# Optimization experiments

Measured on AMD Instinct MI355X. Metric: run time of the kernel, lower is better.

Reference implementation:

```python
import jax, jax.numpy as jnp
import numpy as np


def _topk_masked_softmax(attn, k):
    # Keep only the top-k entries per row (last dim), softmax over them.
    _, idx = jax.lax.top_k(attn, k)  # [b, nh, C, k]
    mask = jnp.put_along_axis(
        jnp.zeros(attn.shape, dtype=bool), idx, True, axis=-1, inplace=False
    )
    return jax.nn.softmax(jnp.where(mask, attn, -jnp.inf), axis=-1)


def setup_inputs() -> dict:
    key = jax.random.key(0)
    k0, k1, k2, k3, k4 = jax.random.split(key, 5)
    b, nh, C = 8, 8, 512
    attn = jax.random.normal(k0, (b, nh, C, C), dtype=jnp.float32)
    # In the torch module these are Parameters initialized to 0.2; use random
    # positive scalars of similar scale for a non-degenerate baseline.
    w1 = jax.random.uniform(k1, (1,), dtype=jnp.float32)
    w2 = jax.random.uniform(k2, (1,), dtype=jnp.float32)
    w3 = jax.random.uniform(k3, (1,), dtype=jnp.float32)
    w4 = jax.random.uniform(k4, (1,), dtype=jnp.float32)
    return {"attn": attn, "w1": w1, "w2": w2, "w3": w3, "w4": w4}


def reference(attn, w1, w2, w3, w4):
    C = attn.shape[-1]
    a1 = _topk_masked_softmax(attn, int(C / 2))
    a2 = _topk_masked_softmax(attn, int(C * 2 / 3))
    a3 = _topk_masked_softmax(attn, int(C * 3 / 4))
    a4 = _topk_masked_softmax(attn, int(C * 4 / 5))
    return a1 * w1 + a2 * w2 + a3 * w3 + a4 * w4
```

## Files before the change

kernel.cpp:

```cpp
#include <hip/hip_runtime.h>
#include <math.h>

#define ROW_C 512
#define NBIN 2048
#define NPACK (NBIN / 2)


static __device__ __forceinline__ unsigned scan64_add(unsigned v) {
    int x = (int)v;
    x += __builtin_amdgcn_update_dpp(0, x, 0x111, 0xF, 0xF, false);
    x += __builtin_amdgcn_update_dpp(0, x, 0x112, 0xF, 0xF, false);
    x += __builtin_amdgcn_update_dpp(0, x, 0x114, 0xF, 0xE, false);
    x += __builtin_amdgcn_update_dpp(0, x, 0x118, 0xF, 0xC, false);
    x += __builtin_amdgcn_update_dpp(0, x, 0x142, 0xA, 0xF, false);
    x += __builtin_amdgcn_update_dpp(0, x, 0x143, 0xC, 0xF, false);
    return (unsigned)x;
}

static __device__ __forceinline__ unsigned scan16_add(unsigned v) {
    int x = (int)v;
    x += __builtin_amdgcn_update_dpp(0, x, 0x111, 0xF, 0xF, false);
    x += __builtin_amdgcn_update_dpp(0, x, 0x112, 0xF, 0xF, false);
    x += __builtin_amdgcn_update_dpp(0, x, 0x114, 0xF, 0xE, false);
    x += __builtin_amdgcn_update_dpp(0, x, 0x118, 0xF, 0xC, false);
    return (unsigned)x;
}

static __device__ __forceinline__ float wave_fadd_red(float v) {
    float t;
    t = __int_as_float(__builtin_amdgcn_update_dpp(0, __float_as_int(v), 0x111, 0xF, 0xF, false)); v += t;
    t = __int_as_float(__builtin_amdgcn_update_dpp(0, __float_as_int(v), 0x112, 0xF, 0xF, false)); v += t;
    t = __int_as_float(__builtin_amdgcn_update_dpp(0, __float_as_int(v), 0x114, 0xF, 0xE, false)); v += t;
    t = __int_as_float(__builtin_amdgcn_update_dpp(0, __float_as_int(v), 0x118, 0xF, 0xC, false)); v += t;
    t = __int_as_float(__builtin_amdgcn_update_dpp(0, __float_as_int(v), 0x142, 0xA, 0xF, false)); v += t;
    t = __int_as_float(__builtin_amdgcn_update_dpp(0, __float_as_int(v), 0x143, 0xC, 0xF, false)); v += t;
    return __int_as_float(__builtin_amdgcn_readlane(__float_as_int(v), 63));
}

static __device__ __forceinline__ float wave_fmax_red(float v) {
    const int NI = (int)0xFF800000;
    float t;
    t = __int_as_float(__builtin_amdgcn_update_dpp(NI, __float_as_int(v), 0x111, 0xF, 0xF, false)); v = fmaxf(v, t);
    t = __int_as_float(__builtin_amdgcn_update_dpp(NI, __float_as_int(v), 0x112, 0xF, 0xF, false)); v = fmaxf(v, t);
    t = __int_as_float(__builtin_amdgcn_update_dpp(NI, __float_as_int(v), 0x114, 0xF, 0xE, false)); v = fmaxf(v, t);
    t = __int_as_float(__builtin_amdgcn_update_dpp(NI, __float_as_int(v), 0x118, 0xF, 0xC, false)); v = fmaxf(v, t);
    t = __int_as_float(__builtin_amdgcn_update_dpp(NI, __float_as_int(v), 0x142, 0xA, 0xF, false)); v = fmaxf(v, t);
    t = __int_as_float(__builtin_amdgcn_update_dpp(NI, __float_as_int(v), 0x143, 0xC, 0xF, false)); v = fmaxf(v, t);
    return __int_as_float(__builtin_amdgcn_readlane(__float_as_int(v), 63));
}

__global__ __launch_bounds__(256) void topk_ms_kernel(
    const float* __restrict__ attn,
    const float* __restrict__ w1p, const float* __restrict__ w2p,
    const float* __restrict__ w3p, const float* __restrict__ w4p,
    float* __restrict__ out)
{
    __shared__ __align__(16) unsigned hist_all[4][NPACK];

    const int lane = threadIdx.x & 63;
    const int wv   = threadIdx.x >> 6;
    unsigned* h = hist_all[wv];
    int4* hv = (int4*)h;

    const long long row  = (long long)blockIdx.x * 4 + wv;
    const long long base = row * ROW_C + lane * 8;

    const float4 A = *reinterpret_cast<const float4*>(attn + base);
    const float4 B = *reinterpret_cast<const float4*>(attn + base + 4);
    float x[8] = {A.x, A.y, A.z, A.w, B.x, B.y, B.z, B.w};

    int bin[8];
    float eo[8];
    #pragma unroll
    for (int s = 0; s < 8; ++s) {
        const float y = __builtin_amdgcn_fmed3f(x[s], -3.90625f, 3.90625f) + 12.0f;
        bin[s] = (int)((__float_as_uint(y) >> 12) & 0x7FFu);
        eo[s] = __expf(x[s]);
    }

    {
        const int4 z = make_int4(0, 0, 0, 0);
        hv[lane] = z; hv[lane + 64] = z; hv[lane + 128] = z; hv[lane + 192] = z;
    }

    #pragma unroll
    for (int s = 0; s < 8; ++s) {
        const int j  = bin[s] >> 1;
        const int ph = j ^ ((j >> 3) & 0x1C);
        atomicAdd(&h[ph], (bin[s] & 1) ? 0x10000u : 1u);
    }

    unsigned ps = 0;
    #pragma unroll
    for (int k = 0; k < 4; ++k) {
        const int b  = 4 * lane + k;
        const int pb = b ^ ((b >> 3) & 7);
        const int4 v = hv[pb];
        ps += (unsigned)v.x + (unsigned)v.y + (unsigned)v.z + (unsigned)v.w;
    }
    const unsigned tot = (ps & 0xFFFFu) + (ps >> 16);

    const unsigned incl = scan64_add(tot);
    const unsigned excl = incl - tot;

    const unsigned long long Ba = __ballot(incl >= 257u);
    const unsigned long long Bb = __ballot(incl >= 172u);
    const unsigned long long Bc = __ballot(incl >= 129u);
    const unsigned long long Bd = __ballot(incl >= 104u);
    const int l0 = __ffsll(Ba) - 1, l1 = __ffsll(Bb) - 1,
              l2 = __ffsll(Bc) - 1, l3 = __ffsll(Bd) - 1;

    const int r = lane >> 4;
    const int lsel = (r == 0) ? l0 : (r == 1) ? l1 : (r == 2) ? l2 : l3;
    const int Tr   = (r == 0) ? 257 : (r == 1) ? 172 : (r == 2) ? 129 : 104;
    const int Kr   = (r == 0) ? 256 : (r == 1) ? 341 : (r == 2) ? 384 : 409;
    const unsigned exl = __shfl(excl, lsel, 64);

    const int jw = (lsel << 4) + (lane & 15);
    const int pw = jw ^ ((jw >> 3) & 0x1C);
    const unsigned w0 = h[pw];
    const unsigned q  = w0 + (w0 << 16);
    const unsigned wt = q >> 16;
    const unsigned sc = scan16_add(wt);
    const unsigned ebase = exl + (sc - wt);
    const int      phi   = (int)(ebase + wt);
    const unsigned long long CB = __ballot(phi >= Tr);
    const int js = __ffs((unsigned)(CB >> (r << 4))) - 1;
    const unsigned q_w  = __shfl(q, (r << 4) + js, 64);
    const unsigned eb_w = __shfl(ebase, (r << 4) + js, 64);

    const int  plo  = (int)(eb_w + (q_w & 0xFFFFu));
    const int  phw  = (int)(eb_w + (q_w >> 16));
    const bool ev   = (plo >= Tr);
    const int  bsel = (((lsel << 4) + js) << 1) + (ev ? 0 : 1);
    const int  locp = ev ? plo : phw;
    const int  prvp = ev ? (int)eb_w : plo;
    const int  Rr   = Kr - 512 + locp;
    const int  alin = (prvp == Tr - 1) ? 1 : 0;
    const unsigned pk = ((unsigned)bsel << 11) | ((unsigned)alin << 10) | (unsigned)Rr;

    int b_[4], R_[4], al_[4]; float tthr[4];
    const float NINF = -__builtin_inff();
    {
        const unsigned v0 = (unsigned)__builtin_amdgcn_readlane((int)pk, 0);
        const unsigned v1 = (unsigned)__builtin_amdgcn_readlane((int)pk, 16);
        const unsigned v2 = (unsigned)__builtin_amdgcn_readlane((int)pk, 32);
        const unsigned v3 = (unsigned)__builtin_amdgcn_readlane((int)pk, 48);
        const unsigned vv[4] = {v0, v1, v2, v3};
        #pragma unroll
        for (int rr = 0; rr < 4; ++rr) {
            b_[rr]  = (int)(vv[rr] >> 11);
            al_[rr] = (int)((vv[rr] >> 10) & 1u);
            R_[rr]  = (int)(vv[rr] & 0x3FFu);
            float t = __uint_as_float((unsigned)(b_[rr] + 0x41000) << 12) - 12.0f;
            tthr[rr] = (b_[rr] <= 24) ? NINF : t;
        }
    }

    int needv[4] = {0,0,0,0}, cntv[4] = {0,0,0,0};
    bool anytb = false;
    #pragma unroll
    for (int rr = 0; rr < 4; ++rr) {
        if (!al_[rr]) {
            float cm[8];
            #pragma unroll
            for (int s = 0; s < 8; ++s)
                cm[s] = (bin[s] == b_[rr]) ? x[s] : NINF;
            int R = R_[rr];
            float t; int c;
            while (true) {
                float mk = cm[0];
                #pragma unroll
                for (int s = 1; s < 8; ++s) mk = fmaxf(mk, cm[s]);
                t = wave_fmax_red(mk);
                c = 0;
                #pragma unroll
                for (int s = 0; s < 8; ++s)
                    c += (int)__popcll(__ballot(cm[s] == t));
                if (c >= R) break;
                R -= c;
                #pragma unroll
                for (int s = 0; s < 8; ++s)
                    cm[s] = (cm[s] == t) ? NINF : cm[s];
            }
            tthr[rr] = t; needv[rr] = R; cntv[rr] = c;
            anytb = anytb || (c != R);
        }
    }

    float res[8];
    if (!anytb) {
        const float t1 = tthr[0], t2 = tthr[1], t3 = tthr[2], t4 = tthr[3];
        float z0 = 0.f, z1 = 0.f, z2 = 0.f, z3 = 0.f;
        #pragma unroll
        for (int s = 0; s < 8; ++s) {
            z0 += (x[s] >= t1) ? eo[s] : 0.f;
            z1 += (x[s] >= t2) ? eo[s] : 0.f;
            z2 += (x[s] >= t3) ? eo[s] : 0.f;
            z3 += (x[s] >= t4) ? eo[s] : 0.f;
        }
        const float Z0 = wave_fadd_red(z0);
        const float Z1 = wave_fadd_red(z1);
        const float Z2 = wave_fadd_red(z2);
        const float Z3 = wave_fadd_red(z3);
        const float wz0 = w1p[0] * __builtin_amdgcn_rcpf(Z0);
        const float wz1 = w2p[0] * __builtin_amdgcn_rcpf(Z1);
        const float wz2 = w3p[0] * __builtin_amdgcn_rcpf(Z2);
        const float wz3 = w4p[0] * __builtin_amdgcn_rcpf(Z3);
        const float u4 = wz3, u3 = u4 + wz2, u2 = u3 + wz1, u1 = u2 + wz0;
        #pragma unroll
        for (int s = 0; s < 8; ++s) {
            float c = (x[s] >= t1) ? u1 : u2;
            c = (x[s] >= t2) ? c : u3;
            c = (x[s] >= t3) ? c : u4;
            c = (x[s] >= t4) ? c : 0.f;
            res[s] = eo[s] * c;
        }
    } else {
        int fl[8] = {0, 0, 0, 0, 0, 0, 0, 0};
        #pragma unroll
        for (int rr = 0; rr < 4; ++rr) {
            const float t = tthr[rr];
            if (al_[rr] || needv[rr] == cntv[rr]) {
                #pragma unroll
                for (int s = 0; s < 8; ++s)
                    fl[s] |= ((int)(x[s] >= t)) << rr;
            } else {
                const unsigned long long ltm = (1ull << lane) - 1ull;
                int basec = 0;
                #pragma unroll
                for (int s = 0; s < 8; ++s)
                    basec += (int)__popcll(__ballot(x[s] == t) & ltm);
                int own = 0;
                #pragma unroll
                for (int s = 0; s < 8; ++s) {
                    const bool eq = (x[s] == t);
                    if (x[s] > t || (eq && (basec + own) < needv[rr]))
                        fl[s] |= (1 << rr);
                    own += eq ? 1 : 0;
                }
            }
        }
        float z0 = 0.f, z1 = 0.f, z2 = 0.f, z3 = 0.f;
        #pragma unroll
        for (int s = 0; s < 8; ++s) {
            z0 += (fl[s] & 1) ? eo[s] : 0.f;
            z1 += (fl[s] & 2) ? eo[s] : 0.f;
            z2 += (fl[s] & 4) ? eo[s] : 0.f;
            z3 += (fl[s] & 8) ? eo[s] : 0.f;
        }
        const float Z0 = wave_fadd_red(z0);
        const float Z1 = wave_fadd_red(z1);
        const float Z2 = wave_fadd_red(z2);
        const float Z3 = wave_fadd_red(z3);
        const float wz0 = w1p[0] * __builtin_amdgcn_rcpf(Z0);
        const float wz1 = w2p[0] * __builtin_amdgcn_rcpf(Z1);
        const float wz2 = w3p[0] * __builtin_amdgcn_rcpf(Z2);
        const float wz3 = w4p[0] * __builtin_amdgcn_rcpf(Z3);
        #pragma unroll
        for (int s = 0; s < 8; ++s) {
            float c = 0.f;
            c += (fl[s] & 1) ? wz0 : 0.f;
            c += (fl[s] & 2) ? wz1 : 0.f;
            c += (fl[s] & 4) ? wz2 : 0.f;
            c += (fl[s] & 8) ? wz3 : 0.f;
            res[s] = eo[s] * c;
        }
    }

    *reinterpret_cast<float4*>(out + base)     = make_float4(res[0], res[1], res[2], res[3]);
    *reinterpret_cast<float4*>(out + base + 4) = make_float4(res[4], res[5], res[6], res[7]);
}

extern "C" void kernel_launch(void* const* d_in, const int* in_sizes, int n_in,
                              void* d_out, int out_size, void* d_ws, size_t ws_size,
                              hipStream_t stream) {
    const float* attn = (const float*)d_in[0];
    const float* w1   = (const float*)d_in[1];
    const float* w2   = (const float*)d_in[2];
    const float* w3   = (const float*)d_in[3];
    const float* w4   = (const float*)d_in[4];
    float* out = (float*)d_out;

    int rows = in_sizes[0] / ROW_C;
    int blocks = (rows + 3) / 4;
    topk_ms_kernel<<<blocks, 256, 0, stream>>>(attn, w1, w2, w3, w4, out);
}
```

Before: 122.3 us.

## Process two rows per wavefront and interleave histogram and threshold phases

```diff
diff --git a/kernel.cpp b/kernel.cpp
--- a/kernel.cpp
+++ b/kernel.cpp
@@ -62,86 +62,93 @@
     unsigned* h = hist_all[wv];
     int4* hv = (int4*)h;
 
-    const long long row  = (long long)blockIdx.x * 4 + wv;
-    const long long base = row * ROW_C + lane * 8;
-
-    const float4 A = *reinterpret_cast<const float4*>(attn + base);
-    const float4 B = *reinterpret_cast<const float4*>(attn + base + 4);
-    float x[8] = {A.x, A.y, A.z, A.w, B.x, B.y, B.z, B.w};
-
-    int bin[8];
-    float eo[8];
-    #pragma unroll
-    for (int s = 0; s < 8; ++s) {
-        const float y = __builtin_amdgcn_fmed3f(x[s], -3.90625f, 3.90625f) + 12.0f;
-        bin[s] = (int)((__float_as_uint(y) >> 12) & 0x7FFu);
-        eo[s] = __expf(x[s]);
+    const long long gid   = (long long)blockIdx.x * 4 + wv;
+    const long long baseA = gid * (2 * ROW_C) + lane * 8;
+    const long long baseB = baseA + ROW_C;
+
+    float xA[8], xB[8];
+    {
+        const float4 A0 = *reinterpret_cast<const float4*>(attn + baseA);
+        const float4 A1 = *reinterpret_cast<const float4*>(attn + baseA + 4);
+        const float4 B0 = *reinterpret_cast<const float4*>(attn + baseB);
+        const float4 B1 = *reinterpret_cast<const float4*>(attn + baseB + 4);
+        xA[0]=A0.x; xA[1]=A0.y; xA[2]=A0.z; xA[3]=A0.w;
+        xA[4]=A1.x; xA[5]=A1.y; xA[6]=A1.z; xA[7]=A1.w;
+        xB[0]=B0.x; xB[1]=B0.y; xB[2]=B0.z; xB[3]=B0.w;
+        xB[4]=B1.x; xB[5]=B1.y; xB[6]=B1.z; xB[7]=B1.w;
     }
 
-    {
+    const float NINF = -__builtin_inff();
+
+    auto BINF = [](float v) -> int {
+        const float y = __builtin_amdgcn_fmed3f(v, -3.90625f, 3.90625f) + 12.0f;
+        return (int)((__float_as_uint(y) >> 12) & 0x7FFu);
+    };
+
+    auto ZERO = [&]() {
         const int4 z = make_int4(0, 0, 0, 0);
         hv[lane] = z; hv[lane + 64] = z; hv[lane + 128] = z; hv[lane + 192] = z;
-    }
-
-    #pragma unroll
-    for (int s = 0; s < 8; ++s) {
-        const int j  = bin[s] >> 1;
-        const int ph = j ^ ((j >> 3) & 0x1C);
-        atomicAdd(&h[ph], (bin[s] & 1) ? 0x10000u : 1u);
-    }
-
-    unsigned ps = 0;
-    #pragma unroll
-    for (int k = 0; k < 4; ++k) {
-        const int b  = 4 * lane + k;
-        const int pb = b ^ ((b >> 3) & 7);
-        const int4 v = hv[pb];
-        ps += (unsigned)v.x + (unsigned)v.y + (unsigned)v.z + (unsigned)v.w;
-    }
-    const unsigned tot = (ps & 0xFFFFu) + (ps >> 16);
-
-    const unsigned incl = scan64_add(tot);
-    const unsigned excl = incl - tot;
-
-    const unsigned long long Ba = __ballot(incl >= 257u);
-    const unsigned long long Bb = __ballot(incl >= 172u);
-    const unsigned long long Bc = __ballot(incl >= 129u);
-    const unsigned long long Bd = __ballot(incl >= 104u);
-    const int l0 = __ffsll(Ba) - 1, l1 = __ffsll(Bb) - 1,
-              l2 = __ffsll(Bc) - 1, l3 = __ffsll(Bd) - 1;
-
-    const int r = lane >> 4;
-    const int lsel = (r == 0) ? l0 : (r == 1) ? l1 : (r == 2) ? l2 : l3;
-    const int Tr   = (r == 0) ? 257 : (r == 1) ? 172 : (r == 2) ? 129 : 104;
-    const int Kr   = (r == 0) ? 256 : (r == 1) ? 341 : (r == 2) ? 384 : 409;
-    const unsigned exl = __shfl(excl, lsel, 64);
-
-    const int jw = (lsel << 4) + (lane & 15);
-    const int pw = jw ^ ((jw >> 3) & 0x1C);
-    const unsigned w0 = h[pw];
-    const unsigned q  = w0 + (w0 << 16);
-    const unsigned wt = q >> 16;
-    const unsigned sc = scan16_add(wt);
-    const unsigned ebase = exl + (sc - wt);
-    const int      phi   = (int)(ebase + wt);
-    const unsigned long long CB = __ballot(phi >= Tr);
-    const int js = __ffs((unsigned)(CB >> (r << 4))) - 1;
-    const unsigned q_w  = __shfl(q, (r << 4) + js, 64);
-    const unsigned eb_w = __shfl(ebase, (r << 4) + js, 64);
-
-    const int  plo  = (int)(eb_w + (q_w & 0xFFFFu));
-    const int  phw  = (int)(eb_w + (q_w >> 16));
-    const bool ev   = (plo >= Tr);
-    const int  bsel = (((lsel << 4) + js) << 1) + (ev ? 0 : 1);
-    const int  locp = ev ? plo : phw;
-    const int  prvp = ev ? (int)eb_w : plo;
-    const int  Rr   = Kr - 512 + locp;
-    const int  alin = (prvp == Tr - 1) ? 1 : 0;
-    const unsigned pk = ((unsigned)bsel << 11) | ((unsigned)alin << 10) | (unsigned)Rr;
-
-    int b_[4], R_[4], al_[4]; float tthr[4];
-    const float NINF = -__builtin_inff();
-    {
+    };
+
+    auto HIST = [&](const float* x) {
+        #pragma unroll
+        for (int s = 0; s < 8; ++s) {
+            const int b  = BINF(x[s]);
+            const int j  = b >> 1;
+            const int ph = j ^ ((j >> 3) & 0x1C);
+            atomicAdd(&h[ph], (b & 1) ? 0x10000u : 1u);
+        }
+    };
+
+    auto FRONT = [&](float* tthr, int* b_, int* R_, int* al_) {
+        unsigned ps = 0;
+        #pragma unroll
+        for (int k = 0; k < 4; ++k) {
+            const int b  = 4 * lane + k;
+            const int pb = b ^ ((b >> 3) & 7);
+            const int4 v = hv[pb];
+            ps += (unsigned)v.x + (unsigned)v.y + (unsigned)v.z + (unsigned)v.w;
+        }
+        const unsigned tot  = (ps & 0xFFFFu) + (ps >> 16);
+        const unsigned incl = scan64_add(tot);
+        const unsigned excl = incl - tot;
+
+        const unsigned long long Ba = __ballot(incl >= 257u);
+        const unsigned long long Bb = __ballot(incl >= 172u);
+        const unsigned long long Bc = __ballot(incl >= 129u);
+        const unsigned long long Bd = __ballot(incl >= 104u);
+        const int l0 = __ffsll(Ba) - 1, l1 = __ffsll(Bb) - 1,
+                  l2 = __ffsll(Bc) - 1, l3 = __ffsll(Bd) - 1;
+
+        const int r = lane >> 4;
+        const int lsel = (r == 0) ? l0 : (r == 1) ? l1 : (r == 2) ? l2 : l3;
+        const int Tr   = (r == 0) ? 257 : (r == 1) ? 172 : (r == 2) ? 129 : 104;
+        const int Kr   = (r == 0) ? 256 : (r == 1) ? 341 : (r == 2) ? 384 : 409;
+        const unsigned exl = __shfl(excl, lsel, 64);
+
+        const int jw = (lsel << 4) + (lane & 15);
+        const int pw = jw ^ ((jw >> 3) & 0x1C);
+        const unsigned w0 = h[pw];
+        const unsigned q  = w0 + (w0 << 16);
+        const unsigned wt = q >> 16;
+        const unsigned sc = scan16_add(wt);
+        const unsigned ebase = exl + (sc - wt);
+        const int      phi   = (int)(ebase + wt);
+        const unsigned long long CB = __ballot(phi >= Tr);
+        const int js = __ffs((unsigned)(CB >> (r << 4))) - 1;
+        const unsigned q_w  = __shfl(q, (r << 4) + js, 64);
+        const unsigned eb_w = __shfl(ebase, (r << 4) + js, 64);
+
+        const int  plo  = (int)(eb_w + (q_w & 0xFFFFu));
+        const int  phw  = (int)(eb_w + (q_w >> 16));
+        const bool ev   = (plo >= Tr);
+        const int  bsel = (((lsel << 4) + js) << 1) + (ev ? 0 : 1);
+        const int  locp = ev ? plo : phw;
+        const int  prvp = ev ? (int)eb_w : plo;
+        const int  Rr   = Kr - 512 + locp;
+        const int  alin = (prvp == Tr - 1) ? 1 : 0;
+        const unsigned pk = ((unsigned)bsel << 11) | ((unsigned)alin << 10) | (unsigned)Rr;
+
         const unsigned v0 = (unsigned)__builtin_amdgcn_readlane((int)pk, 0);
         const unsigned v1 = (unsigned)__builtin_amdgcn_readlane((int)pk, 16);
         const unsigned v2 = (unsigned)__builtin_amdgcn_readlane((int)pk, 32);
@@ -155,121 +162,147 @@
             float t = __uint_as_float((unsigned)(b_[rr] + 0x41000) << 12) - 12.0f;
             tthr[rr] = (b_[rr] <= 24) ? NINF : t;
         }
-    }
-
-    int needv[4] = {0,0,0,0}, cntv[4] = {0,0,0,0};
-    bool anytb = false;
-    #pragma unroll
-    for (int rr = 0; rr < 4; ++rr) {
-        if (!al_[rr]) {
-            float cm[8];
-            #pragma unroll
-            for (int s = 0; s < 8; ++s)
-                cm[s] = (bin[s] == b_[rr]) ? x[s] : NINF;
-            int R = R_[rr];
-            float t; int c;
-            while (true) {
-                float mk = cm[0];
-                #pragma unroll
-                for (int s = 1; s < 8; ++s) mk = fmaxf(mk, cm[s]);
-                t = wave_fmax_red(mk);
-                c = 0;
+    };
+
+    auto BACK = [&](const float* x, float* tthr, const int* b_, const int* R_,
+                    const int* al_, long long obase) {
+        int needv[4] = {0,0,0,0}, cntv[4] = {0,0,0,0};
+        bool anytb = false;
+        const bool needbins = !(al_[0] && al_[1] && al_[2] && al_[3]);
+        int bn[8];
+        if (needbins) {
+            #pragma unroll
+            for (int s = 0; s < 8; ++s) bn[s] = BINF(x[s]);
+        }
+        #pragma unroll
+        for (int rr = 0; rr < 4; ++rr) {
+            if (!al_[rr]) {
+                float cm[8];
                 #pragma unroll
                 for (int s = 0; s < 8; ++s)
-                    c += (int)__popcll(__ballot(cm[s] == t));
-                if (c >= R) break;
-                R -= c;
-                #pragma unroll
-                for (int s = 0; s < 8; ++s)
-                    cm[s] = (cm[s] == t) ? NINF : cm[s];
-            }
-            tthr[rr] = t; needv[rr] = R; cntv[rr] = c;
-            anytb = anytb || (c != R);
-        }
-    }
-
-    float res[8];
-    if (!anytb) {
-        const float t1 = tthr[0], t2 = tthr[1], t3 = tthr[2], t4 = tthr[3];
-        float z0 = 0.f, z1 = 0.f, z2 = 0.f, z3 = 0.f;
-        #pragma unroll
-        for (int s = 0; s < 8; ++s) {
-            z0 += (x[s] >= t1) ? eo[s] : 0.f;
-            z1 += (x[s] >= t2) ? eo[s] : 0.f;
-            z2 += (x[s] >= t3) ? eo[s] : 0.f;
-            z3 += (x[s] >= t4) ? eo[s] : 0.f;
-        }
-        const float Z0 = wave_fadd_red(z0);
-        const float Z1 = wave_fadd_red(z1);
-        const float Z2 = wave_fadd_red(z2);
-        const float Z3 = wave_fadd_red(z3);
-        const float wz0 = w1p[0] * __builtin_amdgcn_rcpf(Z0);
-        const float wz1 = w2p[0] * __builtin_amdgcn_rcpf(Z1);
-        const float wz2 = w3p[0] * __builtin_amdgcn_rcpf(Z2);
-        const float wz3 = w4p[0] * __builtin_amdgcn_rcpf(Z3);
-        const float u4 = wz3, u3 = u4 + wz2, u2 = u3 + wz1, u1 = u2 + wz0;
-        #pragma unroll
-        for (int s = 0; s < 8; ++s) {
-            float c = (x[s] >= t1) ? u1 : u2;
-            c = (x[s] >= t2) ? c : u3;
-            c = (x[s] >= t3) ? c : u4;
-            c = (x[s] >= t4) ? c : 0.f;
-            res[s] = eo[s] * c;
-        }
-    } else {
-        int fl[8] = {0, 0, 0, 0, 0, 0, 0, 0};
-        #pragma unroll
-        for (int rr = 0; rr < 4; ++rr) {
-            const float t = tthr[rr];
-            if (al_[rr] || needv[rr] == cntv[rr]) {
-                #pragma unroll
-                for (int s = 0; s < 8; ++s)
-                    fl[s] |= ((int)(x[s] >= t)) << rr;
-            } else {
-                const unsigned long long ltm = (1ull << lane) - 1ull;
-                int basec = 0;
-                #pragma unroll
-                for (int s = 0; s < 8; ++s)
-                    basec += (int)__popcll(__ballot(x[s] == t) & ltm);
-                int own = 0;
-                #pragma unroll
-                for (int s = 0; s < 8; ++s) {
-                    const bool eq = (x[s] == t);
-                    if (x[s] > t || (eq && (basec + own) < needv[rr]))
-                        fl[s] |= (1 << rr);
-                    own += eq ? 1 : 0;
+                    cm[s] = (bn[s] == b_[rr]) ? x[s] : NINF;
+                int R = R_[rr];
+                float t; int c;
+                while (true) {
+                    float mk = cm[0];
+                    #pragma unroll
+                    for (int s = 1; s < 8; ++s) mk = fmaxf(mk, cm[s]);
+                    t = wave_fmax_red(mk);
+                    c = 0;
+                    #pragma unroll
+                    for (int s = 0; s < 8; ++s)
+                        c += (int)__popcll(__ballot(cm[s] == t));
+                    if (c >= R) break;
+                    R -= c;
+                    #pragma unroll
+                    for (int s = 0; s < 8; ++s)
+                        cm[s] = (cm[s] == t) ? NINF : cm[s];
                 }
-            }
-        }
-        float z0 = 0.f, z1 = 0.f, z2 = 0.f, z3 = 0.f;
-        #pragma unroll
-        for (int s = 0; s < 8; ++s) {
-            z0 += (fl[s] & 1) ? eo[s] : 0.f;
-            z1 += (fl[s] & 2) ? eo[s] : 0.f;
-            z2 += (fl[s] & 4) ? eo[s] : 0.f;
-            z3 += (fl[s] & 8) ? eo[s] : 0.f;
-        }
-        const float Z0 = wave_fadd_red(z0);
-        const float Z1 = wave_fadd_red(z1);
-        const float Z2 = wave_fadd_red(z2);
-        const float Z3 = wave_fadd_red(z3);
-        const float wz0 = w1p[0] * __builtin_amdgcn_rcpf(Z0);
-        const float wz1 = w2p[0] * __builtin_amdgcn_rcpf(Z1);
-        const float wz2 = w3p[0] * __builtin_amdgcn_rcpf(Z2);
-        const float wz3 = w4p[0] * __builtin_amdgcn_rcpf(Z3);
-        #pragma unroll
-        for (int s = 0; s < 8; ++s) {
-            float c = 0.f;
-            c += (fl[s] & 1) ? wz0 : 0.f;
-            c += (fl[s] & 2) ? wz1 : 0.f;
-            c += (fl[s] & 4) ? wz2 : 0.f;
-            c += (fl[s] & 8) ? wz3 : 0.f;
-            res[s] = eo[s] * c;
-        }
-    }
-
-    *reinterpret_cast<float4*>(out + base)     = make_float4(res[0], res[1], res[2], res[3]);
-    *reinterpret_cast<float4*>(out + base + 4) = make_float4(res[4], res[5], res[6], res[7]);
+                tthr[rr] = t; needv[rr] = R; cntv[rr] = c;
+                anytb = anytb || (c != R);
+            }
+        }
+
+        float eo[8];
+        #pragma unroll
+        for (int s = 0; s < 8; ++s) eo[s] = __expf(x[s]);
+
+        float res[8];
+        if (!anytb) {
+            const float t1 = tthr[0], t2 = tthr[1], t3 = tthr[2], t4 = tthr[3];
+            float z0 = 0.f, z1 = 0.f, z2 = 0.f, z3 = 0.f;
+            #pragma unroll
+            for (int s = 0; s < 8; ++s) {
+                z0 += (x[s] >= t1) ? eo[s] : 0.f;
+                z1 += (x[s] >= t2) ? eo[s] : 0.f;
+                z2 += (x[s] >= t3) ? eo[s] : 0.f;
+                z3 += (x[s] >= t4) ? eo[s] : 0.f;
+            }
+            const float Z0 = wave_fadd_red(z0);
+            const float Z1 = wave_fadd_red(z1);
+            const float Z2 = wave_fadd_red(z2);
+            const float Z3 = wave_fadd_red(z3);
+            const float wz0 = w1p[0] * __builtin_amdgcn_rcpf(Z0);
+            const float wz1 = w2p[0] * __builtin_amdgcn_rcpf(Z1);
+            const float wz2 = w3p[0] * __builtin_amdgcn_rcpf(Z2);
+            const float wz3 = w4p[0] * __builtin_amdgcn_rcpf(Z3);
+            const float u4 = wz3, u3 = u4 + wz2, u2 = u3 + wz1, u1 = u2 + wz0;
+            #pragma unroll
+            for (int s = 0; s < 8; ++s) {
+                float c = (x[s] >= t1) ? u1 : u2;
+                c = (x[s] >= t2) ? c : u3;
+                c = (x[s] >= t3) ? c : u4;
+                c = (x[s] >= t4) ? c : 0.f;
+                res[s] = eo[s] * c;
+            }
+        } else {
+            int fl[8] = {0, 0, 0, 0, 0, 0, 0, 0};
+            #pragma unroll
+            for (int rr = 0; rr < 4; ++rr) {
+                const float t = tthr[rr];
+                if (al_[rr] || needv[rr] == cntv[rr]) {
+                    #pragma unroll
+                    for (int s = 0; s < 8; ++s)
+                        fl[s] |= ((int)(x[s] >= t)) << rr;
+                } else {
+                    const unsigned long long ltm = (1ull << lane) - 1ull;
+                    int basec = 0;
+                    #pragma unroll
+                    for (int s = 0; s < 8; ++s)
+                        basec += (int)__popcll(__ballot(x[s] == t) & ltm);
+                    int own = 0;
+                    #pragma unroll
+                    for (int s = 0; s < 8; ++s) {
+                        const bool eq = (x[s] == t);
+                        if (x[s] > t || (eq && (basec + own) < needv[rr]))
+                            fl[s] |= (1 << rr);
+                        own += eq ? 1 : 0;
+                    }
+                }
+            }
+            float z0 = 0.f, z1 = 0.f, z2 = 0.f, z3 = 0.f;
+            #pragma unroll
+            for (int s = 0; s < 8; ++s) {
+                z0 += (fl[s] & 1) ? eo[s] : 0.f;
+                z1 += (fl[s] & 2) ? eo[s] : 0.f;
+                z2 += (fl[s] & 4) ? eo[s] : 0.f;
+                z3 += (fl[s] & 8) ? eo[s] : 0.f;
+            }
+            const float Z0 = wave_fadd_red(z0);
+            const float Z1 = wave_fadd_red(z1);
+            const float Z2 = wave_fadd_red(z2);
+            const float Z3 = wave_fadd_red(z3);
+            const float wz0 = w1p[0] * __builtin_amdgcn_rcpf(Z0);
+            const float wz1 = w2p[0] * __builtin_amdgcn_rcpf(Z1);
+            const float wz2 = w3p[0] * __builtin_amdgcn_rcpf(Z2);
+            const float wz3 = w4p[0] * __builtin_amdgcn_rcpf(Z3);
+            #pragma unroll
+            for (int s = 0; s < 8; ++s) {
+                float c = 0.f;
+                c += (fl[s] & 1) ? wz0 : 0.f;
+                c += (fl[s] & 2) ? wz1 : 0.f;
+                c += (fl[s] & 4) ? wz2 : 0.f;
+                c += (fl[s] & 8) ? wz3 : 0.f;
+                res[s] = eo[s] * c;
+            }
+        }
+
+        *reinterpret_cast<float4*>(out + obase)     = make_float4(res[0], res[1], res[2], res[3]);
+        *reinterpret_cast<float4*>(out + obase + 4) = make_float4(res[4], res[5], res[6], res[7]);
+    };
+
+    ZERO();
+    HIST(xA);
+    float tthrA[4]; int bA[4], RA[4], alA[4];
+    FRONT(tthrA, bA, RA, alA);
+
+    ZERO();
+    HIST(xB);
+
+    BACK(xA, tthrA, bA, RA, alA, baseA);
+    float tthrB[4]; int bB[4], RB[4], alB[4];
+    FRONT(tthrB, bB, RB, alB);
+    BACK(xB, tthrB, bB, RB, alB, baseB);
 }
 
 extern "C" void kernel_launch(void* const* d_in, const int* in_sizes, int n_in,
@@ -282,7 +315,8 @@
     const float* w4   = (const float*)d_in[4];
     float* out = (float*)d_out;
 
-    int rows = in_sizes[0] / ROW_C;
-    int blocks = (rows + 3) / 4;
+    int rows  = in_sizes[0] / ROW_C;
+    int waves = rows / 2;
+    int blocks = (waves + 3) / 4;
     topk_ms_kernel<<<blocks, 256, 0, stream>>>(attn, w1, w2, w3, w4, out);
 }
```

After: 123.4 us. About the same (+0.9%).

## Halve per-row threshold histogram and replace shuffles with readlane broadcasts

Applied to the files above, without the earlier changes.

```diff
diff --git a/kernel.cpp b/kernel.cpp
--- a/kernel.cpp
+++ b/kernel.cpp
@@ -2,7 +2,7 @@
 #include <math.h>
 
 #define ROW_C 512
-#define NBIN 2048
+#define NBIN 1024
 #define NPACK (NBIN / 2)
 
 
@@ -70,36 +70,37 @@
     float x[8] = {A.x, A.y, A.z, A.w, B.x, B.y, B.z, B.w};
 
     int bin[8];
-    float eo[8];
     #pragma unroll
     for (int s = 0; s < 8; ++s) {
-        const float y = __builtin_amdgcn_fmed3f(x[s], -3.90625f, 3.90625f) + 12.0f;
+        const float y = __builtin_amdgcn_fmed3f(x[s], -3.5f, 0.484375f) + 11.5f;
         bin[s] = (int)((__float_as_uint(y) >> 12) & 0x7FFu);
-        eo[s] = __expf(x[s]);
     }
 
     {
         const int4 z = make_int4(0, 0, 0, 0);
-        hv[lane] = z; hv[lane + 64] = z; hv[lane + 128] = z; hv[lane + 192] = z;
+        hv[lane] = z; hv[lane + 64] = z;
     }
 
     #pragma unroll
     for (int s = 0; s < 8; ++s) {
         const int j  = bin[s] >> 1;
-        const int ph = j ^ ((j >> 3) & 0x1C);
+        const int ph = j ^ ((j >> 3) & 0x38);
         atomicAdd(&h[ph], (bin[s] & 1) ? 0x10000u : 1u);
     }
 
     unsigned ps = 0;
-    #pragma unroll
-    for (int k = 0; k < 4; ++k) {
-        const int b  = 4 * lane + k;
-        const int pb = b ^ ((b >> 3) & 7);
+    unsigned wreg[8];
+    #pragma unroll
+    for (int k = 0; k < 2; ++k) {
+        const int Bb = 2 * lane + k;
+        const int pb = Bb ^ ((Bb >> 3) & 0xE);
         const int4 v = hv[pb];
+        wreg[4*k]   = (unsigned)v.x; wreg[4*k+1] = (unsigned)v.y;
+        wreg[4*k+2] = (unsigned)v.z; wreg[4*k+3] = (unsigned)v.w;
         ps += (unsigned)v.x + (unsigned)v.y + (unsigned)v.z + (unsigned)v.w;
     }
-    const unsigned tot = (ps & 0xFFFFu) + (ps >> 16);
-
+    (void)wreg;
+    const unsigned tot  = (ps & 0xFFFFu) + (ps >> 16);
     const unsigned incl = scan64_add(tot);
     const unsigned excl = incl - tot;
 
@@ -110,14 +111,18 @@
     const int l0 = __ffsll(Ba) - 1, l1 = __ffsll(Bb) - 1,
               l2 = __ffsll(Bc) - 1, l3 = __ffsll(Bd) - 1;
 
+    const unsigned e0 = (unsigned)__builtin_amdgcn_readlane((int)excl, l0);
+    const unsigned e1 = (unsigned)__builtin_amdgcn_readlane((int)excl, l1);
+    const unsigned e2 = (unsigned)__builtin_amdgcn_readlane((int)excl, l2);
+    const unsigned e3 = (unsigned)__builtin_amdgcn_readlane((int)excl, l3);
+
     const int r = lane >> 4;
     const int lsel = (r == 0) ? l0 : (r == 1) ? l1 : (r == 2) ? l2 : l3;
     const int Tr   = (r == 0) ? 257 : (r == 1) ? 172 : (r == 2) ? 129 : 104;
-    const int Kr   = (r == 0) ? 256 : (r == 1) ? 341 : (r == 2) ? 384 : 409;
-    const unsigned exl = __shfl(excl, lsel, 64);
-
-    const int jw = (lsel << 4) + (lane & 15);
-    const int pw = jw ^ ((jw >> 3) & 0x1C);
+    const unsigned exl = (r == 0) ? e0 : (r == 1) ? e1 : (r == 2) ? e2 : e3;
+
+    const int jw = ((lsel << 3) + (lane & 15)) & 511;
+    const int pw = jw ^ ((jw >> 3) & 0x38);
     const unsigned w0 = h[pw];
     const unsigned q  = w0 + (w0 << 16);
     const unsigned wt = q >> 16;
@@ -125,35 +130,31 @@
     const unsigned ebase = exl + (sc - wt);
     const int      phi   = (int)(ebase + wt);
     const unsigned long long CB = __ballot(phi >= Tr);
-    const int js = __ffs((unsigned)(CB >> (r << 4))) - 1;
-    const unsigned q_w  = __shfl(q, (r << 4) + js, 64);
-    const unsigned eb_w = __shfl(ebase, (r << 4) + js, 64);
-
-    const int  plo  = (int)(eb_w + (q_w & 0xFFFFu));
-    const int  phw  = (int)(eb_w + (q_w >> 16));
-    const bool ev   = (plo >= Tr);
-    const int  bsel = (((lsel << 4) + js) << 1) + (ev ? 0 : 1);
-    const int  locp = ev ? plo : phw;
-    const int  prvp = ev ? (int)eb_w : plo;
-    const int  Rr   = Kr - 512 + locp;
-    const int  alin = (prvp == Tr - 1) ? 1 : 0;
-    const unsigned pk = ((unsigned)bsel << 11) | ((unsigned)alin << 10) | (unsigned)Rr;
-
+
+    const float NINF = -__builtin_inff();
     int b_[4], R_[4], al_[4]; float tthr[4];
-    const float NINF = -__builtin_inff();
     {
-        const unsigned v0 = (unsigned)__builtin_amdgcn_readlane((int)pk, 0);
-        const unsigned v1 = (unsigned)__builtin_amdgcn_readlane((int)pk, 16);
-        const unsigned v2 = (unsigned)__builtin_amdgcn_readlane((int)pk, 32);
-        const unsigned v3 = (unsigned)__builtin_amdgcn_readlane((int)pk, 48);
-        const unsigned vv[4] = {v0, v1, v2, v3};
+        const int Ls[4] = {l0, l1, l2, l3};
+        const int Ts[4] = {257, 172, 129, 104};
+        const int Ks[4] = {256, 341, 384, 409};
         #pragma unroll
         for (int rr = 0; rr < 4; ++rr) {
-            b_[rr]  = (int)(vv[rr] >> 11);
-            al_[rr] = (int)((vv[rr] >> 10) & 1u);
-            R_[rr]  = (int)(vv[rr] & 0x3FFu);
-            float t = __uint_as_float((unsigned)(b_[rr] + 0x41000) << 12) - 12.0f;
-            tthr[rr] = (b_[rr] <= 24) ? NINF : t;
+            const unsigned cb = (unsigned)(CB >> (rr << 4)) & 0xFFFFu;
+            const int js = __ffs(cb) - 1;
+            const int li = (rr << 4) + js;
+            const unsigned qw  = (unsigned)__builtin_amdgcn_readlane((int)q, li);
+            const unsigned ebw = (unsigned)__builtin_amdgcn_readlane((int)ebase, li);
+            const int  plo  = (int)(ebw + (qw & 0xFFFFu));
+            const int  phw  = (int)(ebw + (qw >> 16));
+            const bool ev   = (plo >= Ts[rr]);
+            const int  bsel = (((Ls[rr] << 3) + js) << 1) + (ev ? 0 : 1);
+            const int  locp = ev ? plo : phw;
+            const int  prvp = ev ? (int)ebw : plo;
+            b_[rr]  = bsel;
+            R_[rr]  = Ks[rr] - 512 + locp;
+            al_[rr] = (prvp == Ts[rr] - 1) ? 1 : 0;
+            const float t = __uint_as_float((unsigned)(bsel + 0x41000) << 12) - 11.5f;
+            tthr[rr] = (bsel < 1) ? NINF : t;
         }
     }
 
@@ -188,6 +189,10 @@
         }
     }
 
+    float eo[8];
+    #pragma unroll
+    for (int s = 0; s < 8; ++s) eo[s] = __expf(x[s]);
+
     float res[8];
     if (!anytb) {
         const float t1 = tthr[0], t2 = tthr[1], t3 = tthr[2], t4 = tthr[3];
```

Measured after the change: 125.4 us. 2.5% more time.
